# Performance work log

Measured on AMD Instinct MI355X. Metric: run time of the kernel, lower is better.

Reference implementation:

```python
import jax, jax.numpy as jnp
import numpy as np

ML_R_PRIORI = 1.5   # mainlobe_window_radius_priori
ML_R_MAX = 4        # mainlobe_window_radius_max
MIN_K = 1           # min_k
ML_WIDTH_POW = 1    # ml_width_pow
DIST_SENTINEL = 100.0


def _grid_offsets(r):
    # all (dy, dx) pairs in [-r, r]^2 -> [(2r+1)^2, 2]
    o = np.arange(-r, r + 1)
    yy, xx = np.meshgrid(o, o, indexing='ij')
    return np.stack([yy.ravel(), xx.ravel()], axis=-1).astype(np.int32)


def setup_inputs() -> dict:
    key = jax.random.key(0)
    B, C, H, W = 256, 324, 18, 18
    k1, k2 = jax.random.split(key)
    cost_volume = jax.random.normal(k1, (B, C, H, W), dtype=jnp.float32)
    peak_coords = jax.random.randint(k2, (B, C, 2), 0, H, dtype=jnp.int32)  # (y, x)
    gy, gx = jnp.meshgrid(jnp.arange(H, dtype=jnp.int32),
                          jnp.arange(W, dtype=jnp.int32), indexing='ij')
    mesh_y = jnp.broadcast_to(gy, (B, C, H, W))
    mesh_x = jnp.broadcast_to(gx, (B, C, H, W))
    return {"cost_volume": cost_volume, "peak_coords": peak_coords,
            "mesh_y": mesh_y, "mesh_x": mesh_x}


def reference(cost_volume, peak_coords, mesh_y, mesh_x):
    B, C, H, W = cost_volume.shape
    BC, HW = B * C, H * W
    cv = cost_volume.reshape(BC, HW)
    peak = peak_coords.reshape(BC, 2)
    my = mesh_y.reshape(BC, HW)
    mx = mesh_x.reshape(BC, HW)

    # --- static offset tables ---
    off_max = jnp.asarray(_grid_offsets(ML_R_MAX))                     # [81, 2]
    off_p = jnp.asarray(_grid_offsets(int(np.ceil(ML_R_PRIORI))))      # [25, 2]
    norm_p = jnp.sqrt(jnp.sum(off_p.astype(jnp.float32) ** 2, -1))
    off_priori = jnp.where((norm_p <= ML_R_PRIORI)[:, None], off_p, 0)  # out-of-radius -> (0,0)

    bidx = jnp.arange(BC)[:, None]

    def scatter_zero_mask(offsets):
        # offsets: [1 or BC, N, 2]; zero out mainlobe window around each peak
        win = peak[:, None, :] + offsets
        wy = jnp.clip(win[..., 0], 0, H - 1)
        wx = jnp.clip(win[..., 1], 0, W - 1)
        flat = wy * W + wx                                  # [BC, N]
        return jnp.ones((BC, HW), jnp.float32).at[bidx, flat].set(0.0)

    # --- priori sidelobe mean ---
    w_pri = scatter_zero_mask(off_priori[None])
    n_pri = w_pri.sum(-1, keepdims=True)
    mean_pri = (cv * w_pri).sum(-1, keepdims=True) / n_pri

    # --- distance to nearest below-mean (sidelobe) point -> mainlobe width ---
    py, px = peak[:, :1], peak[:, 1:]
    dist = jnp.sqrt(((my - py) ** 2 + (mx - px) ** 2).astype(jnp.float32))
    pos = jnp.arange(HW, dtype=jnp.int32)[None]
    peak_flat = py * W + px
    keep = (cv <= mean_pri) & (pos != peak_flat)
    dist = jnp.where(keep, dist, DIST_SENTINEL)
    neg_small, _ = jax.lax.top_k(-dist, MIN_K)              # k smallest distances
    width = (-neg_small).mean(-1, keepdims=True)            # [BC, 1]

    # --- data-dependent mainlobe window (per-row radius) ---
    radius = jnp.clip(width, 1.5, ML_R_MAX + 0.5)           # [BC, 1]
    norms_max = jnp.sqrt(jnp.sum(off_max.astype(jnp.float32) ** 2, -1))  # [81]
    in_r = norms_max[None, :] <= radius                     # [BC, 81]
    off_dyn = jnp.where(in_r[..., None], off_max[None], 0)  # [BC, 81, 2]

    w = scatter_zero_mask(off_dyn)
    n = w.sum(-1, keepdims=True)
    mean_s = (cv * w).sum(-1, keepdims=True) / n
    var_s = (((cv - mean_s) * w) ** 2).sum(-1, keepdims=True) / (n - 1.0)  # use_std_dev=False
    peaks = cv.max(-1, keepdims=True)

    psrw = ((peaks - mean_s) / (var_s * width ** ML_WIDTH_POW + 1e-16)).reshape(B, C)
    saliency = psrw / (psrw.mean(-1, keepdims=True) + 1e-8)
    return saliency
```

## Files before the change

kernel.cpp:

```cpp
#include <hip/hip_runtime.h>
#include <math.h>

constexpr int Hn = 18, Wn = 18, HWn = 324;

__global__ __launch_bounds__(256) void psrw_kernel(
    const float* __restrict__ cv, const int* __restrict__ peak,
    float* __restrict__ out, int BC)
{
    int gtid = blockIdx.x * 256 + threadIdx.x;
    int wave = gtid >> 6;
    int lane = threadIdx.x & 63;
    int g = lane >> 4;
    int l = lane & 15;
    int tile = wave * 4 + g;
    if (tile >= BC) return;

    const float* row = cv + (size_t)tile * HWn;
    int2 pk = ((const int2*)peak)[tile];
    int py = pk.x & 31, px = pk.y & 31;

    const float* colp = row + l;
    float c[21];
#pragma unroll
    for (int j = 0; j < 18; ++j) c[j] = colp[18 * j];
    int lh = l >> 1, lb = l & 1;
    const float* tp = row + (lh * 18 + 16 + lb);
    c[18] = tp[0];
    c[19] = tp[144];
    bool v20 = (l < 4);
    c[20] = v20 ? tp[288] : 0.f;

    float cpk = row[py * Wn + px];

    float m0 = -INFINITY, m1 = -INFINITY, s0 = 0.f, s1 = 0.f;
#pragma unroll
    for (int j = 0; j < 18; j += 2) { m0 = fmaxf(m0, c[j]); s0 += c[j]; }
#pragma unroll
    for (int j = 1; j < 18; j += 2) { m1 = fmaxf(m1, c[j]); s1 += c[j]; }
    m0 = fmaxf(m0, c[18]); s0 += c[18];
    m1 = fmaxf(m1, c[19]); s1 += c[19];
    m0 = fmaxf(m0, v20 ? c[20] : -INFINITY); s0 += c[20];
    float m = fmaxf(m0, m1);
    float s = s0 + s1;

    int ry0 = max(0, py - 1), ry1 = min(Hn - 1, py + 1);
    int rx0 = max(0, px - 1), rx1 = min(Wn - 1, px + 1);
    float rectc = 0.f;
    if (l < 9) {
        int q = (l * 11) >> 5;
        int r = l - 3 * q;
        int ry = ry0 + q, rx = rx0 + r;
        if (ry <= ry1 && rx <= rx1) rectc = row[ry * Wn + rx];
    }
    s -= rectc;
#pragma unroll
    for (int o = 8; o; o >>= 1) {
        s += __shfl_xor(s, o, 64);
        m = fmaxf(m, __shfl_xor(m, o, 64));
    }
    int n_pri = HWn - (ry1 - ry0 + 1) * (rx1 - rx0 + 1);
    float mean_pri = s / (float)n_pri;

    int dxl = l - px;
    int dx2m1 = dxl * dxl - 1;
    unsigned ddm1[21];
    unsigned A = (unsigned)(py * py + dx2m1);
    int Bstep = 1 - 2 * py;
    unsigned dminb = 0xFFFFFFFFu;
#pragma unroll
    for (int j = 0; j < 18; ++j) {
        ddm1[j] = A;
        unsigned t = min(dminb, A);
        dminb = (c[j] <= mean_pri) ? t : dminb;
        A += (unsigned)Bstep;
        Bstep += 2;
    }
    int dyt = lh - py;
    int dxt = 16 + lb - px;
    int dxt2m1 = dxt * dxt - 1;
#pragma unroll
    for (int s2 = 0; s2 < 3; ++s2) {
        int dy = dyt + 8 * s2;
        unsigned dd = (unsigned)(dy * dy + dxt2m1);
        if (s2 == 2 && !v20) dd = 0x7FFFFFFFu;
        ddm1[18 + s2] = dd;
        unsigned t = min(dminb, dd);
        dminb = (c[18 + s2] <= mean_pri) ? t : dminb;
    }
#pragma unroll
    for (int o = 8; o; o >>= 1)
        dminb = min(dminb, (unsigned)__shfl_xor((int)dminb, o, 64));

    float width = (dminb > 577u) ? 100.f
                                 : __builtin_amdgcn_sqrtf((float)(dminb + 1u));
    unsigned rad2m1 = min(max(dminb, 1u), 19u);

    float sd0 = 0.f, sd1 = 0.f, ssd = 0.f;
    int cnt = 0;
#pragma unroll
    for (int j = 0; j < 21; ++j) {
        bool in = (ddm1[j] <= rad2m1);
        float cm = in ? 0.f : c[j];
        if (j & 1) sd1 += cm; else sd0 += cm;
        ssd = fmaf(cm, cm, ssd);
        cnt += in ? 1 : 0;
    }
    float sd = sd0 + sd1;
#pragma unroll
    for (int o = 8; o; o >>= 1) {
        sd  += __shfl_xor(sd, o, 64);
        ssd += __shfl_xor(ssd, o, 64);
        cnt += __shfl_xor(cnt, o, 64);
    }
    sd -= cpk;
    ssd = fmaf(-cpk, cpk, ssd);
    float n = (float)(HWn - 1 - cnt);
    float mean_s = sd * __builtin_amdgcn_rcpf(n);
    float var_s = fmaf(-sd, mean_s, ssd) * __builtin_amdgcn_rcpf(n - 1.f);
    float psrw = (m - mean_s) * __builtin_amdgcn_rcpf(fmaf(var_s, width, 1e-16f));
    if (l == 0) out[tile] = psrw;
}

__global__ __launch_bounds__(256) void norm_kernel(float* __restrict__ out, int B)
{
    int gtid = blockIdx.x * 256 + threadIdx.x;
    int wave = gtid >> 6;
    int lane = threadIdx.x & 63;
    if (wave >= B) return;
    float* row = out + (size_t)wave * HWn;
    float4 v0 = reinterpret_cast<float4*>(row)[lane];
    bool has2 = lane < 17;
    float4 v1 = make_float4(0.f, 0.f, 0.f, 0.f);
    if (has2) v1 = reinterpret_cast<float4*>(row)[64 + lane];
    float s = (v0.x + v0.y) + (v0.z + v0.w) + ((v1.x + v1.y) + (v1.z + v1.w));
#pragma unroll
    for (int o = 32; o; o >>= 1) s += __shfl_xor(s, o, 64);
    float denom = s / 324.0f + 1e-8f;
    v0.x /= denom; v0.y /= denom; v0.z /= denom; v0.w /= denom;
    reinterpret_cast<float4*>(row)[lane] = v0;
    if (has2) {
        v1.x /= denom; v1.y /= denom; v1.z /= denom; v1.w /= denom;
        reinterpret_cast<float4*>(row)[64 + lane] = v1;
    }
}

extern "C" void kernel_launch(void* const* d_in, const int* in_sizes, int n_in,
                              void* d_out, int out_size, void* d_ws, size_t ws_size,
                              hipStream_t stream) {
    const float* cv  = (const float*)d_in[0];
    const int* peak  = (const int*)d_in[1];
    float* out = (float*)d_out;

    int BC = in_sizes[1] / 2;
    int waves = (BC + 3) / 4;
    int blocks1 = (waves + 3) / 4;
    psrw_kernel<<<blocks1, 256, 0, stream>>>(cv, peak, out, BC);

    int B = out_size / HWn;
    int blocks2 = (B + 3) / 4;
    norm_kernel<<<blocks2, 256, 0, stream>>>(out, B);
}
```

Baseline: 25.29 us.

## Fuse PSRW and per-batch normalization into one block-per-batch kernel

Replaces the two-kernel pipeline with a single kernel where each 1024-thread block handles one batch of 324 channels. Per-channel PSRW values go to LDS, are block-reduced, and are normalized in place, which removes the second launch and the global round trip. Each wave processes several tiles with double-buffered register loads so the next tile's loads overlap the current compute. It also recomputes distance values instead of storing a 21-entry array, to cut register use. The trade-off is only 256 blocks of 1024 threads, which lowers parallel granularity and may raise register pressure.

```diff
diff --git a/kernel.cpp b/kernel.cpp
--- a/kernel.cpp
+++ b/kernel.cpp
@@ -2,35 +2,30 @@
 #include <math.h>
 
 constexpr int Hn = 18, Wn = 18, HWn = 324;
+constexpr int CHn = 324;
 
-__global__ __launch_bounds__(256) void psrw_kernel(
-    const float* __restrict__ cv, const int* __restrict__ peak,
-    float* __restrict__ out, int BC)
+__device__ __forceinline__ void load_tile(const float* __restrict__ cvb,
+                                          const int* __restrict__ pkb,
+                                          int t, int l,
+                                          float (&c)[21], int2 &pk)
 {
-    int gtid = blockIdx.x * 256 + threadIdx.x;
-    int wave = gtid >> 6;
-    int lane = threadIdx.x & 63;
-    int g = lane >> 4;
-    int l = lane & 15;
-    int tile = wave * 4 + g;
-    if (tile >= BC) return;
-
-    const float* row = cv + (size_t)tile * HWn;
-    int2 pk = ((const int2*)peak)[tile];
-    int py = pk.x & 31, px = pk.y & 31;
-
+    pk = ((const int2*)pkb)[t];
+    const float* row = cvb + (size_t)t * HWn;
     const float* colp = row + l;
-    float c[21];
 #pragma unroll
     for (int j = 0; j < 18; ++j) c[j] = colp[18 * j];
-    int lh = l >> 1, lb = l & 1;
-    const float* tp = row + (lh * 18 + 16 + lb);
+    const float* tp = row + ((l >> 1) * 18 + 16 + (l & 1));
     c[18] = tp[0];
     c[19] = tp[144];
+    c[20] = (l < 4) ? tp[288] : 0.f;
+}
+
+__device__ __forceinline__ float compute_psrw(const float (&c)[21], int2 pkc,
+                                              int l, const float* __restrict__ row)
+{
+    int py = pkc.x & 31, px = pkc.y & 31;
+    float cpk = row[py * Wn + px];
     bool v20 = (l < 4);
-    c[20] = v20 ? tp[288] : 0.f;
-
-    float cpk = row[py * Wn + px];
 
     float m0 = -INFINITY, m1 = -INFINITY, s0 = 0.f, s1 = 0.f;
 #pragma unroll
@@ -63,27 +58,23 @@
 
     int dxl = l - px;
     int dx2m1 = dxl * dxl - 1;
-    unsigned ddm1[21];
     unsigned A = (unsigned)(py * py + dx2m1);
-    int Bstep = 1 - 2 * py;
+    int Bs = 1 - 2 * py;
     unsigned dminb = 0xFFFFFFFFu;
 #pragma unroll
     for (int j = 0; j < 18; ++j) {
-        ddm1[j] = A;
         unsigned t = min(dminb, A);
         dminb = (c[j] <= mean_pri) ? t : dminb;
-        A += (unsigned)Bstep;
-        Bstep += 2;
+        A += (unsigned)Bs; Bs += 2;
     }
-    int dyt = lh - py;
-    int dxt = 16 + lb - px;
+    int dyt = (l >> 1) - py;
+    int dxt = 16 + (l & 1) - px;
     int dxt2m1 = dxt * dxt - 1;
 #pragma unroll
     for (int s2 = 0; s2 < 3; ++s2) {
         int dy = dyt + 8 * s2;
         unsigned dd = (unsigned)(dy * dy + dxt2m1);
         if (s2 == 2 && !v20) dd = 0x7FFFFFFFu;
-        ddm1[18 + s2] = dd;
         unsigned t = min(dminb, dd);
         dminb = (c[18 + s2] <= mean_pri) ? t : dminb;
     }
@@ -97,11 +88,25 @@
 
     float sd0 = 0.f, sd1 = 0.f, ssd = 0.f;
     int cnt = 0;
+    unsigned A2 = (unsigned)(py * py + dx2m1);
+    int Bs2 = 1 - 2 * py;
 #pragma unroll
-    for (int j = 0; j < 21; ++j) {
-        bool in = (ddm1[j] <= rad2m1);
+    for (int j = 0; j < 18; ++j) {
+        bool in = (A2 <= rad2m1);
         float cm = in ? 0.f : c[j];
         if (j & 1) sd1 += cm; else sd0 += cm;
+        ssd = fmaf(cm, cm, ssd);
+        cnt += in ? 1 : 0;
+        A2 += (unsigned)Bs2; Bs2 += 2;
+    }
+#pragma unroll
+    for (int s2 = 0; s2 < 3; ++s2) {
+        int dy = dyt + 8 * s2;
+        unsigned dd = (unsigned)(dy * dy + dxt2m1);
+        if (s2 == 2 && !v20) dd = 0x7FFFFFFFu;
+        bool in = (dd <= rad2m1);
+        float cm = in ? 0.f : c[18 + s2];
+        if (s2 & 1) sd1 += cm; else sd0 += cm;
         ssd = fmaf(cm, cm, ssd);
         cnt += in ? 1 : 0;
     }
@@ -117,31 +122,64 @@
     float n = (float)(HWn - 1 - cnt);
     float mean_s = sd * __builtin_amdgcn_rcpf(n);
     float var_s = fmaf(-sd, mean_s, ssd) * __builtin_amdgcn_rcpf(n - 1.f);
-    float psrw = (m - mean_s) * __builtin_amdgcn_rcpf(fmaf(var_s, width, 1e-16f));
-    if (l == 0) out[tile] = psrw;
+    return (m - mean_s) * __builtin_amdgcn_rcpf(fmaf(var_s, width, 1e-16f));
 }
 
-__global__ __launch_bounds__(256) void norm_kernel(float* __restrict__ out, int B)
+__global__ __launch_bounds__(1024) void psrw_fused(
+    const float* __restrict__ cv, const int* __restrict__ peak,
+    float* __restrict__ out)
 {
-    int gtid = blockIdx.x * 256 + threadIdx.x;
-    int wave = gtid >> 6;
-    int lane = threadIdx.x & 63;
-    if (wave >= B) return;
-    float* row = out + (size_t)wave * HWn;
-    float4 v0 = reinterpret_cast<float4*>(row)[lane];
-    bool has2 = lane < 17;
-    float4 v1 = make_float4(0.f, 0.f, 0.f, 0.f);
-    if (has2) v1 = reinterpret_cast<float4*>(row)[64 + lane];
-    float s = (v0.x + v0.y) + (v0.z + v0.w) + ((v1.x + v1.y) + (v1.z + v1.w));
+    __shared__ float lds_psrw[CHn];
+    __shared__ float wsum[16];
+    __shared__ float inv_d;
+
+    int b = blockIdx.x;
+    int tid = threadIdx.x;
+    int wid = tid >> 6;
+    int lane = tid & 63;
+    int g = (tid >> 4) & 3;
+    int l = tid & 15;
+
+    const float* cvb = cv + (size_t)b * CHn * HWn;
+    const int*   pkb = peak + (size_t)b * CHn * 2;
+    int lt0 = wid * 4 + g;
+
+    float cA[21], cB[21];
+    int2 pkA, pkB;
+    float blk_sum = 0.f;
+
+    load_tile(cvb, pkb, lt0, l, cA, pkA);
 #pragma unroll
-    for (int o = 32; o; o >>= 1) s += __shfl_xor(s, o, 64);
-    float denom = s / 324.0f + 1e-8f;
-    v0.x /= denom; v0.y /= denom; v0.z /= denom; v0.w /= denom;
-    reinterpret_cast<float4*>(row)[lane] = v0;
-    if (has2) {
-        v1.x /= denom; v1.y /= denom; v1.z /= denom; v1.w /= denom;
-        reinterpret_cast<float4*>(row)[64 + lane] = v1;
+    for (int i = 0; i < 6; i += 2) {
+        if (i + 1 < 6 && (i + 1) * 64 + wid * 4 < CHn)
+            load_tile(cvb, pkb, lt0 + 64 * (i + 1), l, cB, pkB);
+        if (i * 64 + wid * 4 < CHn) {
+            int t = lt0 + 64 * i;
+            float p = compute_psrw(cA, pkA, l, cvb + (size_t)t * HWn);
+            if (l == 0) { lds_psrw[t] = p; blk_sum += p; }
+        }
+        if (i + 2 < 6 && (i + 2) * 64 + wid * 4 < CHn)
+            load_tile(cvb, pkb, lt0 + 64 * (i + 2), l, cA, pkA);
+        if (i + 1 < 6 && (i + 1) * 64 + wid * 4 < CHn) {
+            int t = lt0 + 64 * (i + 1);
+            float p = compute_psrw(cB, pkB, l, cvb + (size_t)t * HWn);
+            if (l == 0) { lds_psrw[t] = p; blk_sum += p; }
+        }
     }
+
+    blk_sum += __shfl_xor(blk_sum, 16, 64);
+    blk_sum += __shfl_xor(blk_sum, 32, 64);
+    if (lane == 0) wsum[wid] = blk_sum;
+    __syncthreads();
+    if (wid == 0) {
+        float v = (lane < 16) ? wsum[lane] : 0.f;
+#pragma unroll
+        for (int o = 8; o; o >>= 1) v += __shfl_xor(v, o, 64);
+        if (lane == 0) inv_d = 1.f / (v / 324.f + 1e-8f);
+    }
+    __syncthreads();
+    float idv = inv_d;
+    if (tid < CHn) out[(size_t)b * CHn + tid] = lds_psrw[tid] * idv;
 }
 
 extern "C" void kernel_launch(void* const* d_in, const int* in_sizes, int n_in,
@@ -151,12 +189,6 @@
     const int* peak  = (const int*)d_in[1];
     float* out = (float*)d_out;
 
-    int BC = in_sizes[1] / 2;
-    int waves = (BC + 3) / 4;
-    int blocks1 = (waves + 3) / 4;
-    psrw_kernel<<<blocks1, 256, 0, stream>>>(cv, peak, out, BC);
-
-    int B = out_size / HWn;
-    int blocks2 = (B + 3) / 4;
-    norm_kernel<<<blocks2, 256, 0, stream>>>(out, B);
+    int B = out_size / CHn;
+    psrw_fused<<<B, 1024, 0, stream>>>(cv, peak, out);
 }
```

Measured after the change: 27.09 us. 1.07x slower.
